# Performance work log

Hardware: AMD Instinct MI355X
Metric: run time of the kernel (lower is better)

## Reference

```python
import jax, jax.numpy as jnp
import numpy as np

C = 512          # in_channels == key_channels
K_REGIONS = 256  # number of proxy/object regions
N, H, Wd = 8, 128, 128


def _cba(x, w, sc, bi):
    """1x1 Conv + (folded) BN + ReLU. x: [n, Cin, h, w], w: [Cout, Cin]."""
    y = jnp.einsum('nchw,oc->nohw', x, w)
    return jax.nn.relu(sc[None, :, None, None] * y + bi[None, :, None, None])


def setup_inputs() -> dict:
    key = jax.random.key(0)
    kx, kp, kw, ks, kb = jax.random.split(key, 5)
    x = jax.random.normal(kx, (N, C, H, Wd), dtype=jnp.float32)
    proxy = jax.random.normal(kp, (N, C, K_REGIONS, 1), dtype=jnp.float32)
    # 7 ConvBnAct layers: [fp0, fp1, fo0, fo1, fd0, fd1, fup]
    W = jax.random.normal(kw, (7, C, C), dtype=jnp.float32) * (1.0 / np.sqrt(C))
    s = jax.random.uniform(ks, (7, C), dtype=jnp.float32, minval=0.5, maxval=1.5)
    b = jax.random.normal(kb, (7, C), dtype=jnp.float32) * 0.02
    return {'x': x, 'proxy': proxy, 'W': W, 's': s, 'b': b}


def reference(x, proxy, W, s, b):
    n, _, h, w = x.shape
    # f_pixel(x): two 1x1 ConvBnAct -> query [n, HW, C]
    q = _cba(_cba(x, W[0], s[0], b[0]), W[1], s[1], b[1])
    query = q.reshape(n, C, h * w).transpose(0, 2, 1)          # [n, HW, C]
    # f_object(proxy) -> key [n, C, K]
    k = _cba(_cba(proxy, W[2], s[2], b[2]), W[3], s[3], b[3])
    key_t = k.reshape(n, C, -1)                                 # [n, C, K]
    # f_down(proxy) -> value [n, K, C]
    v = _cba(_cba(proxy, W[4], s[4], b[4]), W[5], s[5], b[5])
    value = v.reshape(n, C, -1).transpose(0, 2, 1)              # [n, K, C]
    # scaled dot-product attention (single head, unmasked)
    sim = jnp.einsum('nqc,nck->nqk', query, key_t) * (C ** -0.5)
    sim = jax.nn.softmax(sim, axis=-1)                          # [n, HW, K]
    context = jnp.einsum('nqk,nkc->nqc', sim, value)            # [n, HW, C]
    context = context.transpose(0, 2, 1).reshape(n, C, h, w)
    # f_up
    return _cba(context, W[6], s[6], b[6])
```

## Files before the change

kernel.cpp:

```cpp
#include <hip/hip_runtime.h>
#include <hip/hip_bf16.h>
#include <stdint.h>

typedef __bf16 bf16;
typedef __bf16 bf16x8 __attribute__((ext_vector_type(8)));
typedef __bf16 bf16x4v __attribute__((ext_vector_type(4)));
typedef float f32x4 __attribute__((ext_vector_type(4)));

#define AS1 __attribute__((address_space(1)))
#define AS3 __attribute__((address_space(3)))

__device__ __forceinline__ void g2lds16(const bf16* g, bf16* l) {
  __builtin_amdgcn_global_load_lds((AS1 void*)(uintptr_t)g, (AS3 void*)l, 16, 0, 0);
}

__global__ void prep_weights_k(const float* __restrict__ W, const float* __restrict__ s,
                               const float* __restrict__ b, bf16* __restrict__ Wb,
                               float* __restrict__ bb, bf16* __restrict__ W24,
                               float* __restrict__ b24) {
  int idx = blockIdx.x * 256 + threadIdx.x;
  int c = idx & 511;
  int o = (idx >> 9) & 511;
  int l = idx >> 18;
  const float r = 0.04419417382415922f;
  float f = (l == 3) ? r : 1.0f;
  float wv = W[idx] * s[(l << 9) + o] * f;
  float bv = b[(l << 9) + o] * f;
  Wb[idx] = (bf16)wv;
  if (c == 0) bb[(l << 9) + o] = bv;
  if (l == 2) { W24[(size_t)o * 512 + c] = (bf16)wv;         if (c == 0) b24[o] = bv; }
  if (l == 4) { W24[(size_t)(512 + o) * 512 + c] = (bf16)wv; if (c == 0) b24[512 + o] = bv; }
}

__global__ void transpose_cast_k(const float* __restrict__ in, bf16* __restrict__ out,
                                 int R, int S) {
  __shared__ float tile[64][65];
  int s0 = blockIdx.x * 64, r0 = blockIdx.y * 64;
  size_t zo = (size_t)blockIdx.z * R * S;
  int t = threadIdx.x;
  int rr = t >> 4, cc = t & 15;
#pragma unroll
  for (int i = 0; i < 4; i++) {
    float4 v = *(const float4*)&in[zo + (size_t)(r0 + rr + 16 * i) * S + s0 + cc * 4];
    tile[rr + 16 * i][cc * 4 + 0] = v.x;
    tile[rr + 16 * i][cc * 4 + 1] = v.y;
    tile[rr + 16 * i][cc * 4 + 2] = v.z;
    tile[rr + 16 * i][cc * 4 + 3] = v.w;
  }
  __syncthreads();
#pragma unroll
  for (int i = 0; i < 4; i++) {
    int sR = rr + 16 * i;
    bf16x4v o;
    o.x = (bf16)tile[cc * 4 + 0][sR];
    o.y = (bf16)tile[cc * 4 + 1][sR];
    o.z = (bf16)tile[cc * 4 + 2][sR];
    o.w = (bf16)tile[cc * 4 + 3][sR];
    *(bf16x4v*)&out[zo + (size_t)(s0 + sR) * R + r0 + cc * 4] = o;
  }
}

template <bool RELU, bool OUTF32, int BIASMODE>
__global__ __launch_bounds__(256, 2) void gemm_nt(
    const bf16* __restrict__ A, long sAb, int lda,
    const bf16* __restrict__ B, long sBb, int ldb,
    void* __restrict__ OUT, long sOb,
    const float* __restrict__ bias,
    int M, int N, int Kd) {
  __shared__ bf16 sA[128][64];
  __shared__ bf16 sB[128][64];
  const int n0 = blockIdx.x * 128;
  const int m0 = blockIdx.y * 128;
  const bf16* Ab = A + (size_t)blockIdx.z * sAb;
  const bf16* Bb = B + (size_t)blockIdx.z * sBb;
  const int t = threadIdx.x;
  const int lane = t & 63;
  const int w = t >> 6;
  const int wm = (w & 1) << 6;
  const int wn = (w >> 1) << 6;
  const int srow = t >> 3;
  const int scol = (t & 7) << 3;

  f32x4 acc[4][4] = {};
  const int fr = lane & 15;
  const int fq = (lane >> 4) << 3;

  for (int k0 = 0; k0 < Kd; k0 += 64) {
#pragma unroll
    for (int i = 0; i < 4; i++) {
      g2lds16(Ab + (size_t)(m0 + i * 32 + srow) * lda + (k0 + scol), &sA[i * 32 + srow][scol]);
      g2lds16(Bb + (size_t)(n0 + i * 32 + srow) * ldb + (k0 + scol), &sB[i * 32 + srow][scol]);
    }
    __syncthreads();
#pragma unroll
    for (int kk = 0; kk < 64; kk += 32) {
      bf16x8 af[4], bfv[4];
#pragma unroll
      for (int i = 0; i < 4; i++) af[i] = *(const bf16x8*)&sA[wm + i * 16 + fr][kk + fq];
#pragma unroll
      for (int j = 0; j < 4; j++) bfv[j] = *(const bf16x8*)&sB[wn + j * 16 + fr][kk + fq];
#pragma unroll
      for (int i = 0; i < 4; i++)
#pragma unroll
        for (int j = 0; j < 4; j++)
          acc[i][j] = __builtin_amdgcn_mfma_f32_16x16x32_bf16(af[i], bfv[j], acc[i][j], 0, 0, 0);
    }
    __syncthreads();
  }

  const int rb = m0 + wm + ((lane >> 4) << 2);
  const int cb = n0 + wn + (lane & 15);
#pragma unroll
  for (int i = 0; i < 4; i++) {
#pragma unroll
    for (int r = 0; r < 4; r++) {
      const int orow = rb + i * 16 + r;
#pragma unroll
      for (int j = 0; j < 4; j++) {
        const int oc = cb + j * 16;
        float vv = acc[i][j][r];
        if (BIASMODE == 1) vv += bias[oc];
        else if (BIASMODE == 2) vv += bias[orow];
        if (RELU) vv = fmaxf(vv, 0.0f);
        if (OUTF32)
          ((float*)OUT)[(size_t)blockIdx.z * sOb + (size_t)orow * N + oc] = vv;
        else
          ((bf16*)OUT)[(size_t)blockIdx.z * sOb + (size_t)orow * N + oc] = (bf16)vv;
      }
    }
  }
}

__global__ __launch_bounds__(256, 2) void flash_attn_k(
    const bf16* __restrict__ Q, const bf16* __restrict__ Key,
    const bf16* __restrict__ V, bf16* __restrict__ CTX) {
  __shared__ char smraw[65536];
  bf16 (*sq)[64]    = (bf16(*)[64])smraw;
  bf16 (*skey)[64]  = (bf16(*)[64])(smraw + 8192);
  bf16 (*sP)[256]   = (bf16(*)[256])smraw;
  bf16 (*sv)[256]   = (bf16(*)[256])(smraw + 32768);

  const int t = threadIdx.x;
  const int lane = t & 63;
  const int w = t >> 6;
  const int m0 = blockIdx.x * 64;
  const size_t zq = (size_t)blockIdx.y * 16384 * 512;
  const size_t zk = (size_t)blockIdx.y * 256 * 512;
  const bf16* Qz = Q + zq;
  const bf16* Kz = Key + zk;
  const bf16* Vz = V + zk;
  bf16* Cz = CTX + zq;

  const int fr = lane & 15;
  const int quad = lane >> 4;
  const int fq = quad << 3;

  f32x4 accS[16] = {};
  {
    const int srow = t >> 3;
    const int scol = (t & 7) << 3;
    for (int k0 = 0; k0 < 512; k0 += 64) {
#pragma unroll
      for (int i = 0; i < 2; i++)
        g2lds16(Qz + (size_t)(m0 + i * 32 + srow) * 512 + k0 + scol, &sq[i * 32 + srow][scol]);
#pragma unroll
      for (int i = 0; i < 8; i++)
        g2lds16(Kz + (size_t)(i * 32 + srow) * 512 + k0 + scol, &skey[i * 32 + srow][scol]);
      __syncthreads();
#pragma unroll
      for (int kk = 0; kk < 64; kk += 32) {
        bf16x8 aq = *(const bf16x8*)&sq[w * 16 + fr][kk + fq];
#pragma unroll
        for (int j = 0; j < 16; j++) {
          bf16x8 bk = *(const bf16x8*)&skey[j * 16 + fr][kk + fq];
          accS[j] = __builtin_amdgcn_mfma_f32_16x16x32_bf16(aq, bk, accS[j], 0, 0, 0);
        }
      }
      __syncthreads();
    }
  }

#pragma unroll
  for (int r = 0; r < 4; r++) {
    float m = accS[0][r];
#pragma unroll
    for (int j = 1; j < 16; j++) m = fmaxf(m, accS[j][r]);
#pragma unroll
    for (int o = 1; o < 16; o <<= 1) m = fmaxf(m, __shfl_xor(m, o));
    float sum = 0.0f;
#pragma unroll
    for (int j = 0; j < 16; j++) { float e = __expf(accS[j][r] - m); accS[j][r] = e; sum += e; }
#pragma unroll
    for (int o = 1; o < 16; o <<= 1) sum += __shfl_xor(sum, o);
    float inv = 1.0f / sum;
#pragma unroll
    for (int j = 0; j < 16; j++) accS[j][r] *= inv;
  }

#pragma unroll
  for (int j = 0; j < 16; j++)
#pragma unroll
    for (int r = 0; r < 4; r++)
      sP[w * 16 + quad * 4 + r][j * 16 + fr] = (bf16)accS[j][r];

  {
    const int srow = t >> 5;
    const int scol = (t & 31) << 3;
    for (int c0 = 0; c0 < 512; c0 += 64) {
#pragma unroll
      for (int i = 0; i < 8; i++)
        g2lds16(Vz + (size_t)(c0 + i * 8 + srow) * 256 + scol, &sv[i * 8 + srow][scol]);
      __syncthreads();
      f32x4 accC[4] = {};
#pragma unroll
      for (int kk = 0; kk < 256; kk += 32) {
        bf16x8 ap = *(const bf16x8*)&sP[w * 16 + fr][kk + fq];
#pragma unroll
        for (int j = 0; j < 4; j++) {
          bf16x8 bv = *(const bf16x8*)&sv[j * 16 + fr][kk + fq];
          accC[j] = __builtin_amdgcn_mfma_f32_16x16x32_bf16(ap, bv, accC[j], 0, 0, 0);
        }
      }
#pragma unroll
      for (int j = 0; j < 4; j++)
#pragma unroll
        for (int r = 0; r < 4; r++)
          Cz[(size_t)(m0 + w * 16 + quad * 4 + r) * 512 + c0 + j * 16 + fr] = (bf16)accC[j][r];
      __syncthreads();
    }
  }
}

extern "C" void kernel_launch(void* const* d_in, const int* in_sizes, int n_in,
                              void* d_out, int out_size, void* d_ws, size_t ws_size,
                              hipStream_t stream) {
  const float* x = (const float*)d_in[0];
  const float* proxy = (const float*)d_in[1];
  const float* W = (const float*)d_in[2];
  const float* s = (const float*)d_in[3];
  const float* b = (const float*)d_in[4];
  float* out = (float*)d_out;

  const int C = 512, K = 256, NB = 8, HW = 16384;
  const size_t MiB = 1024 * 1024;
  char* ws = (char*)d_ws;
  if (ws_size < 272 * MiB) return;

  bf16* Wb   = (bf16*)(ws + 0);
  float* bb  = (float*)(ws + 3670016);
  bf16* W24  = (bf16*)(ws + 4 * MiB);
  float* b24 = (float*)(ws + 5 * MiB);
  bf16* pT   = (bf16*)(ws + 6 * MiB);
  bf16* kt   = (bf16*)(ws + 8 * MiB);
  bf16* key  = (bf16*)(ws + 12 * MiB);
  bf16* v    = (bf16*)(ws + 14 * MiB);
  bf16* bufA = (bf16*)(ws + 16 * MiB);
  bf16* bufB = (bf16*)(ws + 144 * MiB);

  bf16* xb  = bufA;
  bf16* t0  = bufB;
  bf16* q   = bufA;
  bf16* ctx = bufB;

  const long KC = (long)K * C;
  const long KT = (long)K * 1024;
  const long HWC = (long)HW * C;

  prep_weights_k<<<7 * 512 * 512 / 256, 256, 0, stream>>>(W, s, b, Wb, bb, W24, b24);
  transpose_cast_k<<<dim3(K / 64, C / 64, NB), 256, 0, stream>>>(proxy, pT, C, K);
  transpose_cast_k<<<dim3(HW / 64, C / 64, NB), 256, 0, stream>>>(x, xb, C, HW);
  gemm_nt<true, false, 1><<<dim3(1024 / 128, K / 128, NB), 256, 0, stream>>>(
      pT, KC, C, W24, 0, C, kt, KT, b24, K, 1024, C);
  gemm_nt<true, false, 1><<<dim3(C / 128, K / 128, NB), 256, 0, stream>>>(
      kt, KT, 1024, Wb + 3 * 262144, 0, C, key, KC, bb + 3 * 512, K, C, C);
  gemm_nt<true, false, 2><<<dim3(K / 128, C / 128, NB), 256, 0, stream>>>(
      Wb + 5 * 262144, 0, C, kt + 512, KT, 1024, v, KC, bb + 5 * 512, C, K, C);
  gemm_nt<true, false, 1><<<dim3(C / 128, HW / 128, NB), 256, 0, stream>>>(
      xb, HWC, C, Wb, 0, C, t0, HWC, bb, HW, C, C);
  gemm_nt<true, false, 1><<<dim3(C / 128, HW / 128, NB), 256, 0, stream>>>(
      t0, HWC, C, Wb + 1 * 262144, 0, C, q, HWC, bb + 512, HW, C, C);
  flash_attn_k<<<dim3(HW / 64, NB), 256, 0, stream>>>(q, key, v, ctx);
  gemm_nt<true, true, 2><<<dim3(HW / 128, C / 128, NB), 256, 0, stream>>>(
      Wb + 6 * 262144, 0, C, ctx, HWC, C, out, HWC, bb + 6 * 512, C, HW, C);
}
```

Before: 1.080 ms.

## Split fused attention into sim-softmax kernel plus separate P·V GEMM

Replaces the fused attention kernel with a QK^T+softmax kernel that handles 128 query rows per block (two 16-row MFMA tiles per wave, reusing each key fragment twice) and writes the bf16 probability matrix P to global memory. The P·V product is then done by the existing tiled gemm_nt kernel, and ctx is moved into bufA. This aims to improve key reuse and MFMA efficiency over the small 64-row fused tiles, at the cost of a 64 MiB round trip of P through global memory and one extra launch.

Result: faster. 956.9 us (-11.4%).

```diff
diff --git a/kernel.cpp b/kernel.cpp
--- a/kernel.cpp
+++ b/kernel.cpp
@@ -131,102 +131,72 @@
   }
 }
 
-__global__ __launch_bounds__(256, 2) void flash_attn_k(
-    const bf16* __restrict__ Q, const bf16* __restrict__ Key,
-    const bf16* __restrict__ V, bf16* __restrict__ CTX) {
-  __shared__ char smraw[65536];
-  bf16 (*sq)[64]    = (bf16(*)[64])smraw;
-  bf16 (*skey)[64]  = (bf16(*)[64])(smraw + 8192);
-  bf16 (*sP)[256]   = (bf16(*)[256])smraw;
-  bf16 (*sv)[256]   = (bf16(*)[256])(smraw + 32768);
-
+__global__ __launch_bounds__(256, 2) void sim_softmax_k(
+    const bf16* __restrict__ Q, const bf16* __restrict__ Key, bf16* __restrict__ P) {
+  __shared__ bf16 sQ[128][64];
+  __shared__ bf16 sK[256][64];
   const int t = threadIdx.x;
   const int lane = t & 63;
   const int w = t >> 6;
-  const int m0 = blockIdx.x * 64;
-  const size_t zq = (size_t)blockIdx.y * 16384 * 512;
-  const size_t zk = (size_t)blockIdx.y * 256 * 512;
-  const bf16* Qz = Q + zq;
-  const bf16* Kz = Key + zk;
-  const bf16* Vz = V + zk;
-  bf16* Cz = CTX + zq;
+  const int m0 = blockIdx.x * 128;
+  const bf16* Qz = Q + (size_t)blockIdx.y * 16384 * 512;
+  const bf16* Kz = Key + (size_t)blockIdx.y * 256 * 512;
+  bf16* Pz = P + (size_t)blockIdx.y * 16384 * 256;
 
   const int fr = lane & 15;
   const int quad = lane >> 4;
   const int fq = quad << 3;
-
-  f32x4 accS[16] = {};
-  {
-    const int srow = t >> 3;
-    const int scol = (t & 7) << 3;
-    for (int k0 = 0; k0 < 512; k0 += 64) {
-#pragma unroll
-      for (int i = 0; i < 2; i++)
-        g2lds16(Qz + (size_t)(m0 + i * 32 + srow) * 512 + k0 + scol, &sq[i * 32 + srow][scol]);
-#pragma unroll
-      for (int i = 0; i < 8; i++)
-        g2lds16(Kz + (size_t)(i * 32 + srow) * 512 + k0 + scol, &skey[i * 32 + srow][scol]);
-      __syncthreads();
-#pragma unroll
-      for (int kk = 0; kk < 64; kk += 32) {
-        bf16x8 aq = *(const bf16x8*)&sq[w * 16 + fr][kk + fq];
-#pragma unroll
-        for (int j = 0; j < 16; j++) {
-          bf16x8 bk = *(const bf16x8*)&skey[j * 16 + fr][kk + fq];
-          accS[j] = __builtin_amdgcn_mfma_f32_16x16x32_bf16(aq, bk, accS[j], 0, 0, 0);
-        }
+  const int wm = w << 5;
+  const int srow = t >> 3;
+  const int scol = (t & 7) << 3;
+
+  f32x4 acc[2][16] = {};
+
+  for (int k0 = 0; k0 < 512; k0 += 64) {
+#pragma unroll
+    for (int i = 0; i < 4; i++)
+      g2lds16(Qz + (size_t)(m0 + i * 32 + srow) * 512 + k0 + scol, &sQ[i * 32 + srow][scol]);
+#pragma unroll
+    for (int i = 0; i < 8; i++)
+      g2lds16(Kz + (size_t)(i * 32 + srow) * 512 + k0 + scol, &sK[i * 32 + srow][scol]);
+    __syncthreads();
+#pragma unroll
+    for (int kk = 0; kk < 64; kk += 32) {
+      bf16x8 aq0 = *(const bf16x8*)&sQ[wm + fr][kk + fq];
+      bf16x8 aq1 = *(const bf16x8*)&sQ[wm + 16 + fr][kk + fq];
+#pragma unroll
+      for (int j = 0; j < 16; j++) {
+        bf16x8 bk = *(const bf16x8*)&sK[j * 16 + fr][kk + fq];
+        acc[0][j] = __builtin_amdgcn_mfma_f32_16x16x32_bf16(aq0, bk, acc[0][j], 0, 0, 0);
+        acc[1][j] = __builtin_amdgcn_mfma_f32_16x16x32_bf16(aq1, bk, acc[1][j], 0, 0, 0);
       }
-      __syncthreads();
-    }
-  }
-
-#pragma unroll
-  for (int r = 0; r < 4; r++) {
-    float m = accS[0][r];
-#pragma unroll
-    for (int j = 1; j < 16; j++) m = fmaxf(m, accS[j][r]);
-#pragma unroll
-    for (int o = 1; o < 16; o <<= 1) m = fmaxf(m, __shfl_xor(m, o));
-    float sum = 0.0f;
-#pragma unroll
-    for (int j = 0; j < 16; j++) { float e = __expf(accS[j][r] - m); accS[j][r] = e; sum += e; }
-#pragma unroll
-    for (int o = 1; o < 16; o <<= 1) sum += __shfl_xor(sum, o);
-    float inv = 1.0f / sum;
-#pragma unroll
-    for (int j = 0; j < 16; j++) accS[j][r] *= inv;
-  }
-
-#pragma unroll
-  for (int j = 0; j < 16; j++)
-#pragma unroll
-    for (int r = 0; r < 4; r++)
-      sP[w * 16 + quad * 4 + r][j * 16 + fr] = (bf16)accS[j][r];
-
-  {
-    const int srow = t >> 5;
-    const int scol = (t & 31) << 3;
-    for (int c0 = 0; c0 < 512; c0 += 64) {
-#pragma unroll
-      for (int i = 0; i < 8; i++)
-        g2lds16(Vz + (size_t)(c0 + i * 8 + srow) * 256 + scol, &sv[i * 8 + srow][scol]);
-      __syncthreads();
-      f32x4 accC[4] = {};
-#pragma unroll
-      for (int kk = 0; kk < 256; kk += 32) {
-        bf16x8 ap = *(const bf16x8*)&sP[w * 16 + fr][kk + fq];
-#pragma unroll
-        for (int j = 0; j < 4; j++) {
-          bf16x8 bv = *(const bf16x8*)&sv[j * 16 + fr][kk + fq];
-          accC[j] = __builtin_amdgcn_mfma_f32_16x16x32_bf16(ap, bv, accC[j], 0, 0, 0);
-        }
+    }
+    __syncthreads();
+  }
+
+#pragma unroll
+  for (int i = 0; i < 2; i++) {
+#pragma unroll
+    for (int r = 0; r < 4; r++) {
+      float m = acc[i][0][r];
+#pragma unroll
+      for (int j = 1; j < 16; j++) m = fmaxf(m, acc[i][j][r]);
+#pragma unroll
+      for (int o = 1; o < 16; o <<= 1) m = fmaxf(m, __shfl_xor(m, o));
+      float sum = 0.0f;
+#pragma unroll
+      for (int j = 0; j < 16; j++) {
+        float e = __expf(acc[i][j][r] - m);
+        acc[i][j][r] = e;
+        sum += e;
       }
 #pragma unroll
-      for (int j = 0; j < 4; j++)
-#pragma unroll
-        for (int r = 0; r < 4; r++)
-          Cz[(size_t)(m0 + w * 16 + quad * 4 + r) * 512 + c0 + j * 16 + fr] = (bf16)accC[j][r];
-      __syncthreads();
+      for (int o = 1; o < 16; o <<= 1) sum += __shfl_xor(sum, o);
+      float inv = 1.0f / sum;
+      const size_t rowoff = (size_t)(m0 + wm + i * 16 + (quad << 2) + r) * 256;
+#pragma unroll
+      for (int j = 0; j < 16; j++)
+        Pz[rowoff + j * 16 + fr] = (bf16)(acc[i][j][r] * inv);
     }
   }
 }
@@ -260,11 +230,13 @@
   bf16* xb  = bufA;
   bf16* t0  = bufB;
   bf16* q   = bufA;
-  bf16* ctx = bufB;
+  bf16* P   = bufB;
+  bf16* ctx = bufA;
 
   const long KC = (long)K * C;
   const long KT = (long)K * 1024;
   const long HWC = (long)HW * C;
+  const long HWK = (long)HW * K;
 
   prep_weights_k<<<7 * 512 * 512 / 256, 256, 0, stream>>>(W, s, b, Wb, bb, W24, b24);
   transpose_cast_k<<<dim3(K / 64, C / 64, NB), 256, 0, stream>>>(proxy, pT, C, K);
@@ -279,7 +251,9 @@
       xb, HWC, C, Wb, 0, C, t0, HWC, bb, HW, C, C);
   gemm_nt<true, false, 1><<<dim3(C / 128, HW / 128, NB), 256, 0, stream>>>(
       t0, HWC, C, Wb + 1 * 262144, 0, C, q, HWC, bb + 512, HW, C, C);
-  flash_attn_k<<<dim3(HW / 64, NB), 256, 0, stream>>>(q, key, v, ctx);
+  sim_softmax_k<<<dim3(HW / 128, NB), 256, 0, stream>>>(q, key, P);
+  gemm_nt<false, false, 0><<<dim3(C / 128, HW / 128, NB), 256, 0, stream>>>(
+      P, HWK, K, v, KC, K, ctx, HWC, nullptr, HW, C, K);
   gemm_nt<true, true, 2><<<dim3(HW / 128, C / 128, NB), 256, 0, stream>>>(
       Wb + 6 * 262144, 0, C, ctx, HWC, C, out, HWC, bb + 6 * 512, C, HW, C);
 }
```
